# Performance work log

Hardware: AMD Instinct MI355X
Metric: run time of the kernel (lower is better)

The kernel has to match this reference:

```python
import jax, jax.numpy as jnp
import numpy as np

HEADS = 16
DIM_HEAD = 64
SCALE = DIM_HEAD ** -0.5
EPS = 1e-5


def _vdp_linear(mu, sigma, Wmu, Wsig_raw):
    # y = W x with W ~ N(Wmu, softplus(Wsig_raw)), x ~ N(mu, sigma) (diag covs):
    # Var(y) = (mu^2 + sigma) @ Wsig^T + sigma @ (Wmu^2)^T
    Wsig = jax.nn.softplus(Wsig_raw)
    mu_y = mu @ Wmu.T
    sigma_y = (mu * mu + sigma) @ Wsig.T + sigma @ (Wmu * Wmu).T
    return mu_y, sigma_y


def _vdp_layernorm(mu, sigma, gamma, beta):
    mean = jnp.mean(mu, axis=-1, keepdims=True)
    var = jnp.var(mu, axis=-1, keepdims=True)
    inv = 1.0 / jnp.sqrt(var + EPS)
    mu_y = (mu - mean) * inv * gamma + beta
    # first-order variance propagation through the affine normalization
    sigma_y = sigma * (gamma * gamma) * (inv * inv)
    return mu_y, sigma_y


def _vdp_softmax(mu, sigma):
    p = jax.nn.softmax(mu, axis=-1)
    # diagonal-Jacobian approximation: J_ii = p_i(1-p_i)
    J = p * (1.0 - p)
    return p, (J * J) * sigma


def setup_inputs() -> dict:
    key = jax.random.key(0)
    ks = jax.random.split(key, 6)
    B, N, D = 4, 1024, 1024
    inner = HEADS * DIM_HEAD  # 1024
    w_std = 0.02
    return {
        "mu": jax.random.normal(ks[0], (B, N, D), jnp.float32),
        "sigma": jax.random.uniform(ks[1], (B, N, D), jnp.float32),
        "ln_gamma": jnp.ones((D,), jnp.float32),
        "ln_beta": jnp.zeros((D,), jnp.float32),
        "Wqkv_mu": w_std * jax.random.normal(ks[2], (3 * inner, D), jnp.float32),
        "Wqkv_sigma_raw": -5.0 + 0.1 * jax.random.normal(ks[3], (3 * inner, D), jnp.float32),
        "Wout_mu": w_std * jax.random.normal(ks[4], (D, inner), jnp.float32),
        "Wout_sigma_raw": -5.0 + 0.1 * jax.random.normal(ks[5], (D, inner), jnp.float32),
    }


def reference(mu, sigma, ln_gamma, ln_beta, Wqkv_mu, Wqkv_sigma_raw, Wout_mu, Wout_sigma_raw):
    B, N, D = mu.shape

    mu_n, sigma_n = _vdp_layernorm(mu, sigma, ln_gamma, ln_beta)
    mu_qkv, sigma_qkv = _vdp_linear(mu_n, sigma_n, Wqkv_mu, Wqkv_sigma_raw)

    def split_heads(t):
        q, k, v = jnp.split(t, 3, axis=-1)
        rs = lambda a: a.reshape(B, N, HEADS, DIM_HEAD).transpose(0, 2, 1, 3)
        return rs(q), rs(k), rs(v)

    mu_q, mu_k, mu_v = split_heads(mu_qkv)
    sg_q, sg_k, sg_v = split_heads(sigma_qkv)

    mu_dots = jnp.einsum("bhid,bhjd->bhij", mu_q, mu_k) * SCALE
    sg_dots = jnp.einsum("bhid,bhjd->bhij", sg_q, sg_k) * SCALE

    mu_attn, sg_attn = _vdp_softmax(mu_dots, sg_dots)

    mu_o = jnp.einsum("bhij,bhjd->bhid", mu_attn, mu_v)
    sg_o = jnp.einsum("bhij,bhjd->bhid", sg_attn, sg_v)

    merge = lambda t: t.transpose(0, 2, 1, 3).reshape(B, N, HEADS * DIM_HEAD)
    mu_o, sg_o = merge(mu_o), merge(sg_o)

    return _vdp_linear(mu_o, sg_o, Wout_mu, Wout_sigma_raw)
```

## Files before the change

kernel.cpp:

```cpp
#include <hip/hip_runtime.h>

typedef unsigned short u16;
typedef unsigned int u32;
typedef __bf16 bf16x8 __attribute__((ext_vector_type(8)));
typedef float f32x4 __attribute__((ext_vector_type(4)));
typedef float f32x16 __attribute__((ext_vector_type(16)));

__device__ __forceinline__ float b2f(u16 u) { return __uint_as_float(((u32)u) << 16); }
__device__ __forceinline__ u16 f2b(float f) {
  u32 u = __float_as_uint(f);
  u += 0x7fffu + ((u >> 16) & 1u);
  return (u16)(u >> 16);
}

__device__ __forceinline__ void gll16(const u16* g, u16* l) {
  __builtin_amdgcn_global_load_lds(
      (const __attribute__((address_space(1))) void*)g,
      (__attribute__((address_space(3))) void*)l, 16, 0, 0);
}

__device__ __forceinline__ float4 load4(const void* p, size_t idx, bool f32) {
  if (f32) return *(const float4*)((const float*)p + idx);
  ushort4 u = *(const ushort4*)((const u16*)p + idx);
  return make_float4(b2f(u.x), b2f(u.y), b2f(u.z), b2f(u.w));
}

__global__ __launch_bounds__(256) void detect_kernel(const u16* __restrict__ sig,
                                                     int* __restrict__ flag) {
  __shared__ int cnt;
  if (threadIdx.x == 0) cnt = 0;
  __syncthreads();
  int c = 0;
  for (int i = threadIdx.x; i < 16384; i += 256) {
    u16 v = sig[i];
    c += ((v & 0x7F80u) == 0x7F80u) ? 1 : 0;
  }
  atomicAdd(&cnt, c);
  __syncthreads();
  if (threadIdx.x == 0) *flag = (cnt >= 8) ? 1 : 0;
}

__global__ __launch_bounds__(256) void ln_prep_kernel(
    const int* __restrict__ flag,
    const void* __restrict__ mu, const void* __restrict__ sigma,
    const void* __restrict__ gamma, const void* __restrict__ beta,
    u16* __restrict__ mu_n, u16* __restrict__ a1sg)
{
  __shared__ float ps[4], pq[4];
  const bool f32 = (*flag != 0);
  const int t = threadIdx.x;
  const int wv = t >> 6, lane = t & 63;
  const size_t base = (size_t)blockIdx.x * 1024 + (size_t)t * 4;
  float4 xm = load4(mu, base, f32);
  float4 xs = load4(sigma, base, f32);
  float x0 = xm.x, x1 = xm.y, x2 = xm.z, x3 = xm.w;
  float s0 = xs.x, s1 = xs.y, s2 = xs.z, s3 = xs.w;

  float sv = x0 + x1 + x2 + x3;
  float qv = x0*x0 + x1*x1 + x2*x2 + x3*x3;
  #pragma unroll
  for (int off = 32; off > 0; off >>= 1) {
    sv += __shfl_xor(sv, off, 64);
    qv += __shfl_xor(qv, off, 64);
  }
  if (lane == 0) { ps[wv] = sv; pq[wv] = qv; }
  __syncthreads();
  float sum = ps[0] + ps[1] + ps[2] + ps[3];
  float ssq = pq[0] + pq[1] + pq[2] + pq[3];

  float mean = sum * (1.0f / 1024.0f);
  float var  = ssq * (1.0f / 1024.0f) - mean * mean;
  float inv  = 1.0f / sqrtf(var + 1e-5f);
  float inv2 = inv * inv;

  float4 g4 = load4(gamma, (size_t)t * 4, f32);
  float4 b4 = load4(beta, (size_t)t * 4, f32);

  float m0 = (x0 - mean) * inv * g4.x + b4.x;
  float m1 = (x1 - mean) * inv * g4.y + b4.y;
  float m2 = (x2 - mean) * inv * g4.z + b4.z;
  float m3 = (x3 - mean) * inv * g4.w + b4.w;
  float v0 = s0 * g4.x * g4.x * inv2;
  float v1 = s1 * g4.y * g4.y * inv2;
  float v2 = s2 * g4.z * g4.z * inv2;
  float v3 = s3 * g4.w * g4.w * inv2;

  ushort4 omu = { f2b(m0), f2b(m1), f2b(m2), f2b(m3) };
  ushort4 oa1 = { f2b(m0*m0 + v0), f2b(m1*m1 + v1), f2b(m2*m2 + v2), f2b(m3*m3 + v3) };
  ushort4 osg = { f2b(v0), f2b(v1), f2b(v2), f2b(v3) };
  *(ushort4*)(mu_n + base) = omu;
  size_t r2 = (size_t)blockIdx.x * 2048 + (size_t)t * 4;
  *(ushort4*)(a1sg + r2) = oa1;
  *(ushort4*)(a1sg + r2 + 1024) = osg;
}

__global__ __launch_bounds__(256) void wprep_kernel(
    const int* __restrict__ flag,
    const void* __restrict__ wq_mu, const void* __restrict__ wq_sraw,
    u16* __restrict__ q_bf, u16* __restrict__ q_s2,
    const void* __restrict__ wo_mu, const void* __restrict__ wo_sraw,
    u16* __restrict__ o_bf, u16* __restrict__ o_s2, int nq)
{
  const bool f32 = (*flag != 0);
  size_t idx = ((size_t)blockIdx.x * 256 + threadIdx.x) * 4;
  const void *wmu, *wsr; u16 *obf, *os2;
  if (idx < (size_t)nq) { wmu = wq_mu; wsr = wq_sraw; obf = q_bf; os2 = q_s2; }
  else { idx -= nq; wmu = wo_mu; wsr = wo_sraw; obf = o_bf; os2 = o_s2; }
  int row = (int)(idx >> 10), k = (int)(idx & 1023);
  float4 m4 = load4(wmu, idx, f32);
  float4 s4 = load4(wsr, idx, f32);
  float m[4] = { m4.x, m4.y, m4.z, m4.w };
  float s[4] = { s4.x, s4.y, s4.z, s4.w };
  ushort4 ob, os, oq;
  u16* obp = (u16*)&ob; u16* osp = (u16*)&os; u16* oqp = (u16*)&oq;
  #pragma unroll
  for (int i = 0; i < 4; ++i) {
    float sp = (s[i] > 15.f) ? s[i] : log1pf(__expf(s[i]));
    obp[i] = f2b(m[i]);
    osp[i] = f2b(sp);
    oqp[i] = f2b(m[i] * m[i]);
  }
  *(ushort4*)(obf + idx) = ob;
  size_t r2 = (size_t)row * 2048 + k;
  *(ushort4*)(os2 + r2) = os;
  *(ushort4*)(os2 + r2 + 1024) = oq;
}

template<bool DYN>
__global__ __launch_bounds__(256, 4) void gemm_pair_kernel(
    const u16* __restrict__ A0, const u16* __restrict__ B0, int K0, void* C0, size_t ob0,
    const u16* __restrict__ A1, const u16* __restrict__ B1, int K1, void* C1, size_t ob1,
    int split, int N, const int* __restrict__ flag)
{
  __shared__ u16 lA[128 * 64];
  __shared__ u16 lB[128 * 64];
  const int t = threadIdx.x;
  int bx = blockIdx.x;
  const u16 *A, *B; void* C; size_t obase; int K;
  if (bx < split) { A = A0; B = B0; K = K0; C = C0; obase = ob0; }
  else { bx -= split; A = A1; B = B1; K = K1; C = C1; obase = ob1; }

  const int n0 = bx * 128, m0 = blockIdx.y * 128;
  const int lane = t & 63, wave = t >> 6;
  const int wr = (wave >> 1) * 64, wc = (wave & 1) * 64;
  const int m31 = lane & 31, h5 = lane >> 5;
  const int mx = m31 & 7;

  const int srow = t >> 3;
  const int gseg = (t & 7) ^ (srow & 7);

  f32x16 acc[2][2];
  #pragma unroll
  for (int i = 0; i < 2; ++i)
    #pragma unroll
    for (int j = 0; j < 2; ++j)
      #pragma unroll
      for (int r = 0; r < 16; ++r) acc[i][j][r] = 0.f;

  for (int k0 = 0; k0 < K; k0 += 64) {
    __syncthreads();
    #pragma unroll
    for (int rep = 0; rep < 4; ++rep) {
      gll16(A + (size_t)(m0 + srow + rep * 32) * K + k0 + gseg * 8,
            lA + rep * 2048 + wave * 512);
      gll16(B + (size_t)(n0 + srow + rep * 32) * K + k0 + gseg * 8,
            lB + rep * 2048 + wave * 512);
    }
    __syncthreads();
    #pragma unroll
    for (int ks = 0; ks < 4; ++ks) {
      const int seg = ks * 2 + h5;
      bf16x8 af[2], bfr[2];
      #pragma unroll
      for (int tm = 0; tm < 2; ++tm)
        af[tm] = *(const bf16x8*)&lA[(wr + tm * 32 + m31) * 64 + (seg ^ mx) * 8];
      #pragma unroll
      for (int tn = 0; tn < 2; ++tn)
        bfr[tn] = *(const bf16x8*)&lB[(wc + tn * 32 + m31) * 64 + (seg ^ mx) * 8];
      #pragma unroll
      for (int tm = 0; tm < 2; ++tm)
        #pragma unroll
        for (int tn = 0; tn < 2; ++tn)
          acc[tm][tn] = __builtin_amdgcn_mfma_f32_32x32x16_bf16(af[tm], bfr[tn], acc[tm][tn], 0, 0, 0);
    }
  }

  const bool of32 = DYN && (*flag != 0);
  #pragma unroll
  for (int tm = 0; tm < 2; ++tm)
    #pragma unroll
    for (int tn = 0; tn < 2; ++tn) {
      int colb = n0 + wc + tn * 32 + m31;
      #pragma unroll
      for (int r = 0; r < 16; ++r) {
        int row = m0 + wr + tm * 32 + (r & 3) + 8 * (r >> 2) + 4 * h5;
        float v = acc[tm][tn][r];
        size_t off = obase + (size_t)row * N + colb;
        if (DYN) {
          if (of32) ((float*)C)[off] = v;
          else      ((u16*)C)[off] = f2b(v);
        } else {
          ((u16*)C)[off] = f2b(v);
        }
      }
    }
}

#define SB __builtin_amdgcn_sched_barrier(0)
#define BARRIER do { SB; __builtin_amdgcn_s_barrier(); SB; } while (0)

__global__ __launch_bounds__(512, 2) void gemm8_pair_kernel(
    const u16* __restrict__ A0, const u16* __restrict__ B0, int K0, u16* __restrict__ C0,
    const u16* __restrict__ A1, const u16* __restrict__ B1, int K1, u16* __restrict__ C1,
    int split, int N)
{
  __shared__ u16 lA[2 * 2 * 128 * 64];
  __shared__ u16 lB[2 * 2 * 128 * 64];
  const int t = threadIdx.x;
  int bx = blockIdx.x;
  const u16 *A, *B; u16* C; int K;
  if (bx < split) { A = A0; B = B0; K = K0; C = C0; }
  else { bx -= split; A = A1; B = B1; K = K1; C = C1; }
  const int NT = K >> 6;
  const int n0 = bx * 256, m0 = blockIdx.y * 256;
  const int lane = t & 63, wave = t >> 6;
  const int wm = wave >> 2, wn = wave & 3;
  const int ml = lane & 15, qd = lane >> 4, mx = ml & 7;

  auto stg = [&](const u16* __restrict__ X, int row0, int k0, u16* ldsHalf) {
    #pragma unroll
    for (int j = 0; j < 2; ++j) {
      int r = (wave * 2 + j) * 8 + (lane >> 3);
      int seg = (lane & 7) ^ ((lane >> 3) & 7);
      gll16(X + (size_t)(row0 + r) * K + k0 + seg * 8,
            ldsHalf + (wave * 2 + j) * 512);
    }
  };

  const u16* rdA = lA + (wm * 128 + ml) * 64;
  const u16* rdB = lB + ((wn >> 1) * 128 + (wn & 1) * 64 + ml) * 64;

  f32x4 acc[8][4];
  #pragma unroll
  for (int i = 0; i < 8; ++i)
    #pragma unroll
    for (int j = 0; j < 4; ++j)
      acc[i][j] = (f32x4){0.f, 0.f, 0.f, 0.f};

  bf16x8 fa[4][2];
  bf16x8 fb[2][2][2];

  stg(A, m0,       0,  lA);
  stg(A, m0 + 128, 0,  lA + 8192);
  stg(B, n0,       0,  lB);
  stg(B, n0 + 128, 0,  lB + 8192);
  if (NT > 1) {
    stg(B, n0,       64, lB + 16384);
    stg(B, n0 + 128, 64, lB + 16384 + 8192);
  }
  SB;
  asm volatile("s_waitcnt vmcnt(4)" ::: "memory");
  BARRIER;

  for (int T = 0; T < NT; ++T) {
    const int bo  = (T & 1) * 16384;
    const int bon = bo ^ 16384;
    const int kn  = (T + 1) * 64;
    const int kn2 = (T + 2) * 64;

    #pragma unroll
    for (int i = 0; i < 4; ++i)
      #pragma unroll
      for (int ks = 0; ks < 2; ++ks)
        fa[i][ks] = *(const bf16x8*)&rdA[bo + i * 1024 + ((ks * 4 + qd) ^ mx) * 8];
    #pragma unroll
    for (int j = 0; j < 2; ++j)
      #pragma unroll
      for (int ks = 0; ks < 2; ++ks)
        fb[0][j][ks] = *(const bf16x8*)&rdB[bo + j * 1024 + ((ks * 4 + qd) ^ mx) * 8];
    if (T + 1 < NT) stg(A, m0, kn, lA + bon);
    BARRIER;
    __builtin_amdgcn_s_setprio(1);
    #pragma unroll
    for (int i = 0; i < 4; ++i)
      #pragma unroll
      for (int j = 0; j < 2; ++j)
        #pragma unroll
        for (int ks = 0; ks < 2; ++ks)
          acc[i][j] = __builtin_amdgcn_mfma_f32_16x16x32_bf16(fa[i][ks], fb[0][j][ks], acc[i][j], 0, 0, 0);
    __builtin_amdgcn_s_setprio(0);
    BARRIER;

    #pragma unroll
    for (int j = 0; j < 2; ++j)
      #pragma unroll
      for (int ks = 0; ks < 2; ++ks)
        fb[1][j][ks] = *(const bf16x8*)&rdB[bo + (2 + j) * 1024 + ((ks * 4 + qd) ^ mx) * 8];
    if (T + 1 < NT) stg(A, m0 + 128, kn, lA + bon + 8192);
    BARRIER;
    __builtin_amdgcn_s_setprio(1);
    #pragma unroll
    for (int i = 0; i < 4; ++i)
      #pragma unroll
      for (int j = 0; j < 2; ++j)
        #pragma unroll
        for (int ks = 0; ks < 2; ++ks)
          acc[i][2 + j] = __builtin_amdgcn_mfma_f32_16x16x32_bf16(fa[i][ks], fb[1][j][ks], acc[i][2 + j], 0, 0, 0);
    __builtin_amdgcn_s_setprio(0);
    BARRIER;

    #pragma unroll
    for (int i = 0; i < 4; ++i)
      #pragma unroll
      for (int ks = 0; ks < 2; ++ks)
        fa[i][ks] = *(const bf16x8*)&rdA[bo + (4 + i) * 1024 + ((ks * 4 + qd) ^ mx) * 8];
    if (T + 2 < NT) stg(B, n0, kn2, lB + bo);
    BARRIER;
    __builtin_amdgcn_s_setprio(1);
    #pragma unroll
    for (int i = 0; i < 4; ++i)
      #pragma unroll
      for (int j = 0; j < 2; ++j)
        #pragma unroll
        for (int ks = 0; ks < 2; ++ks)
          acc[4 + i][2 + j] = __builtin_amdgcn_mfma_f32_16x16x32_bf16(fa[i][ks], fb[1][j][ks], acc[4 + i][2 + j], 0, 0, 0);
    __builtin_amdgcn_s_setprio(0);
    BARRIER;

    if (T + 2 < NT) stg(B, n0 + 128, kn2, lB + bo + 8192);
    BARRIER;
    __builtin_amdgcn_s_setprio(1);
    #pragma unroll
    for (int i = 0; i < 4; ++i)
      #pragma unroll
      for (int j = 0; j < 2; ++j)
        #pragma unroll
        for (int ks = 0; ks < 2; ++ks)
          acc[4 + i][j] = __builtin_amdgcn_mfma_f32_16x16x32_bf16(fa[i][ks], fb[0][j][ks], acc[4 + i][j], 0, 0, 0);
    __builtin_amdgcn_s_setprio(0);
    SB;
    if (T + 2 < NT) asm volatile("s_waitcnt vmcnt(4)" ::: "memory");
    else            asm volatile("s_waitcnt vmcnt(0)" ::: "memory");
    BARRIER;
  }

  #pragma unroll
  for (int mf = 0; mf < 8; ++mf)
    #pragma unroll
    for (int nf = 0; nf < 4; ++nf)
      #pragma unroll
      for (int r = 0; r < 4; ++r) {
        int row = m0 + wm * 128 + mf * 16 + qd * 4 + r;
        int col = n0 + wn * 64 + nf * 16 + ml;
        C[(size_t)row * N + col] = f2b(acc[mf][nf][r]);
      }
}

__global__ __launch_bounds__(256) void attn_pass1(
    const u16* __restrict__ qkv_mu, float* __restrict__ invl)
{
  __shared__ u16 lK[128 * 72];
  const int t = threadIdx.x;
  const int wv = t >> 6, lane = t & 63;
  const int ml = lane & 15, qd = lane >> 4;
  const int bh = blockIdx.y;
  const int b = bh >> 4, h = bh & 15;
  const size_t rowbase = (size_t)b * 1024 * 3072;
  const int i0 = blockIdx.x * 64;
  const int qcol = h * 64, kcol = 1024 + h * 64;
  const int qrow = wv * 16;

  bf16x8 aQm[2];
  #pragma unroll
  for (int ks = 0; ks < 2; ++ks)
    aQm[ks] = *(const bf16x8*)(qkv_mu + rowbase +
        (size_t)(i0 + qrow + ml) * 3072 + qcol + ks * 32 + qd * 8);

  float lsum[4] = {0.f, 0.f, 0.f, 0.f};

  for (int j0 = 0; j0 < 1024; j0 += 128) {
    __syncthreads();
    #pragma unroll
    for (int rep = 0; rep < 4; ++rep) {
      int c = t + rep * 256;
      int row = c >> 3, seg = c & 7;
      *(uint4*)&lK[row * 72 + seg * 8] =
          *(const uint4*)(qkv_mu + rowbase + (size_t)(j0 + row) * 3072 + kcol + seg * 8);
    }
    __syncthreads();
    #pragma unroll
    for (int tj = 0; tj < 8; ++tj) {
      bf16x8 b0 = *(const bf16x8*)&lK[(tj * 16 + ml) * 72 + qd * 8];
      bf16x8 b1 = *(const bf16x8*)&lK[(tj * 16 + ml) * 72 + 32 + qd * 8];
      f32x4 s = (f32x4){0.f, 0.f, 0.f, 0.f};
      s = __builtin_amdgcn_mfma_f32_16x16x32_bf16(aQm[0], b0, s, 0, 0, 0);
      s = __builtin_amdgcn_mfma_f32_16x16x32_bf16(aQm[1], b1, s, 0, 0, 0);
      #pragma unroll
      for (int r = 0; r < 4; ++r) lsum[r] += __expf(s[r] * 0.125f);
    }
  }
  #pragma unroll
  for (int r = 0; r < 4; ++r) {
    float l = lsum[r];
    #pragma unroll
    for (int xo = 1; xo < 16; xo <<= 1) l += __shfl_xor(l, xo, 64);
    if (ml == 0)
      invl[(size_t)bh * 1024 + i0 + qrow + qd * 4 + r] = 1.0f / l;
  }
}

__global__ __launch_bounds__(512, 4) void attn_pass2(
    const u16* __restrict__ qkv_mu, const u16* __restrict__ qkv_sg,
    const float* __restrict__ invl,
    u16* __restrict__ o_mu, u16* __restrict__ a1sgo)
{
  __shared__ u16 lKW[128 * 72];
  __shared__ u16 lV[128 * 72];
  __shared__ u16 lP[128 * 72];
  __shared__ u16 lW[128 * 72];

  const int t = threadIdx.x;
  const int wv = t >> 6, lane = t & 63;
  const int ml = lane & 15, qd = lane >> 4;
  const int bh = blockIdx.y;
  const int b = bh >> 4, h = bh & 15;
  const size_t rowbase = (size_t)b * 1024 * 3072;
  const int i0 = blockIdx.x * 128;
  const int qcol = h * 64, kcol = 1024 + h * 64, vcol = 2048 + h * 64;
  const int qrow = wv * 16;

  bf16x8 aQm[2], aQs[2];
  #pragma unroll
  for (int ks = 0; ks < 2; ++ks) {
    size_t ga = rowbase + (size_t)(i0 + qrow + ml) * 3072 + qcol + ks * 32 + qd * 8;
    aQm[ks] = *(const bf16x8*)(qkv_mu + ga);
    aQs[ks] = *(const bf16x8*)(qkv_sg + ga);
  }

  float lacc[4];
  #pragma unroll
  for (int r = 0; r < 4; ++r)
    lacc[r] = invl[(size_t)bh * 1024 + i0 + qrow + qd * 4 + r];

  f32x4 accm[4], accs[4];
  #pragma unroll
  for (int tj = 0; tj < 4; ++tj) {
    accm[tj] = (f32x4){0.f, 0.f, 0.f, 0.f};
    accs[tj] = (f32x4){0.f, 0.f, 0.f, 0.f};
  }

  for (int j0 = 0; j0 < 1024; j0 += 64) {
    __syncthreads();
    #pragma unroll
    for (int rep = 0; rep < 2; ++rep) {
      int c = t + rep * 512;
      int row = c >> 3, seg = c & 7;
      const u16* src = (row < 64) ? qkv_mu : qkv_sg;
      int rr = row & 63;
      *(uint4*)&lKW[row * 72 + seg * 8] =
          *(const uint4*)(src + rowbase + (size_t)(j0 + rr) * 3072 + kcol + seg * 8);
    }
    {
      int buf = t >> 8, rem = t & 255;
      int db = rem >> 4, tb = rem & 15;
      const u16* src = buf ? qkv_sg : qkv_mu;
      ushort4 vals[4];
      #pragma unroll
      for (int i = 0; i < 4; ++i)
        vals[i] = *(const ushort4*)(src + rowbase + (size_t)(j0 + tb * 4 + i) * 3072 + vcol + db * 4);
      #pragma unroll
      for (int k = 0; k < 4; ++k) {
        ushort4 o;
        u16* op = (u16*)&o;
        const u16* v0 = (const u16*)&vals[0];
        const u16* v1 = (const u16*)&vals[1];
        const u16* v2 = (const u16*)&vals[2];
        const u16* v3 = (const u16*)&vals[3];
        op[0] = v0[k]; op[1] = v1[k]; op[2] = v2[k]; op[3] = v3[k];
        *(ushort4*)&lV[(buf * 64 + db * 4 + k) * 72 + tb * 4] = o;
      }
    }
    __syncthreads();

    f32x4 sm[4], ss[4];
    #pragma unroll
    for (int tj = 0; tj < 4; ++tj) {
      bf16x8 bm0 = *(const bf16x8*)&lKW[(tj * 16 + ml) * 72 + qd * 8];
      bf16x8 bm1 = *(const bf16x8*)&lKW[(tj * 16 + ml) * 72 + 32 + qd * 8];
      bf16x8 bs0 = *(const bf16x8*)&lKW[(64 + tj * 16 + ml) * 72 + qd * 8];
      bf16x8 bs1 = *(const bf16x8*)&lKW[(64 + tj * 16 + ml) * 72 + 32 + qd * 8];
      f32x4 s = (f32x4){0.f, 0.f, 0.f, 0.f};
      s = __builtin_amdgcn_mfma_f32_16x16x32_bf16(aQm[0], bm0, s, 0, 0, 0);
      s = __builtin_amdgcn_mfma_f32_16x16x32_bf16(aQm[1], bm1, s, 0, 0, 0);
      sm[tj] = s;
      f32x4 s2 = (f32x4){0.f, 0.f, 0.f, 0.f};
      s2 = __builtin_amdgcn_mfma_f32_16x16x32_bf16(aQs[0], bs0, s2, 0, 0, 0);
      s2 = __builtin_amdgcn_mfma_f32_16x16x32_bf16(aQs[1], bs1, s2, 0, 0, 0);
      ss[tj] = s2;
    }

    #pragma unroll
    for (int tj = 0; tj < 4; ++tj)
      #pragma unroll
      for (int r = 0; r < 4; ++r) {
        float p = __expf(sm[tj][r] * 0.125f) * lacc[r];
        float jp = p * (1.0f - p);
        float w = jp * jp * (ss[tj][r] * 0.125f);
        int row = qrow + qd * 4 + r;
        lP[row * 72 + tj * 16 + ml] = f2b(p);
        lW[row * 72 + tj * 16 + ml] = f2b(w);
      }
    __syncthreads();

    bf16x8 ap[2], aw[2];
    #pragma unroll
    for (int ks = 0; ks < 2; ++ks) {
      ap[ks] = *(const bf16x8*)&lP[(qrow + ml) * 72 + ks * 32 + qd * 8];
      aw[ks] = *(const bf16x8*)&lW[(qrow + ml) * 72 + ks * 32 + qd * 8];
    }
    #pragma unroll
    for (int tj = 0; tj < 4; ++tj) {
      bf16x8 vm0 = *(const bf16x8*)&lV[(tj * 16 + ml) * 72 + qd * 8];
      bf16x8 vm1 = *(const bf16x8*)&lV[(tj * 16 + ml) * 72 + 32 + qd * 8];
      bf16x8 vs0 = *(const bf16x8*)&lV[(64 + tj * 16 + ml) * 72 + qd * 8];
      bf16x8 vs1 = *(const bf16x8*)&lV[(64 + tj * 16 + ml) * 72 + 32 + qd * 8];
      accm[tj] = __builtin_amdgcn_mfma_f32_16x16x32_bf16(ap[0], vm0, accm[tj], 0, 0, 0);
      accm[tj] = __builtin_amdgcn_mfma_f32_16x16x32_bf16(ap[1], vm1, accm[tj], 0, 0, 0);
      accs[tj] = __builtin_amdgcn_mfma_f32_16x16x32_bf16(aw[0], vs0, accs[tj], 0, 0, 0);
      accs[tj] = __builtin_amdgcn_mfma_f32_16x16x32_bf16(aw[1], vs1, accs[tj], 0, 0, 0);
    }
  }

  #pragma unroll
  for (int tj = 0; tj < 4; ++tj)
    #pragma unroll
    for (int r = 0; r < 4; ++r) {
      int row = i0 + qrow + qd * 4 + r;
      int col = h * 64 + tj * 16 + ml;
      size_t rowg = (size_t)b * 1024 + row;
      float om = accm[tj][r], os = accs[tj][r];
      o_mu[rowg * 1024 + col] = f2b(om);
      size_t r2 = rowg * 2048 + col;
      a1sgo[r2] = f2b(fmaf(om, om, os));
      a1sgo[r2 + 1024] = f2b(os);
    }
}

extern "C" void kernel_launch(void* const* d_in, const int* in_sizes, int n_in,
                              void* d_out, int out_size, void* d_ws, size_t ws_size,
                              hipStream_t stream)
{
  (void)in_sizes; (void)n_in; (void)out_size; (void)ws_size;
  const void* mu        = d_in[0];
  const void* sigma     = d_in[1];
  const void* gamma     = d_in[2];
  const void* beta      = d_in[3];
  const void* wqkv_mu   = d_in[4];
  const void* wqkv_sraw = d_in[5];
  const void* wout_mu   = d_in[6];
  const void* wout_sraw = d_in[7];

  u16* ws = (u16*)d_ws;
  const size_t R = 4096;
  u16* mu_n   = ws;
  u16* a1sg   = mu_n + R * 1024;
  u16* wq_bf  = a1sg + R * 2048;
  u16* wqs2   = wq_bf + 3072 * 1024;
  u16* wo_bf  = wqs2 + 3072 * 2048;
  u16* wos2   = wo_bf + 1024 * 1024;
  u16* mu_qkv = wos2 + 1024 * 2048;
  u16* sg_qkv = mu_qkv + R * 3072;
  int* flag   = (int*)(sg_qkv + R * 3072);
  float* invl = (float*)(flag + 16);

  u16* mu_o  = mu_n;
  u16* a1sgo = a1sg;

  detect_kernel<<<1, 256, 0, stream>>>((const u16*)sigma, flag);
  ln_prep_kernel<<<4096, 256, 0, stream>>>(flag, mu, sigma, gamma, beta, mu_n, a1sg);
  wprep_kernel<<<(4 * 1024 * 1024) / 1024, 256, 0, stream>>>(
      flag, wqkv_mu, wqkv_sraw, wq_bf, wqs2,
      wout_mu, wout_sraw, wo_bf, wos2, 3072 * 1024);

  gemm8_pair_kernel<<<dim3(24, 16), 512, 0, stream>>>(
      mu_n, wq_bf, 1024, mu_qkv,
      a1sg, wqs2, 2048, sg_qkv,
      12, 3072);

  attn_pass1<<<dim3(16, 64), 256, 0, stream>>>(mu_qkv, invl);
  attn_pass2<<<dim3(8, 64), 512, 0, stream>>>(mu_qkv, sg_qkv, invl, mu_o, a1sgo);

  gemm_pair_kernel<true><<<dim3(16, 32), 256, 0, stream>>>(
      mu_o, wo_bf, 1024, d_out, 0,
      a1sgo, wos2, 2048, d_out, R * 1024,
      8, 1024, flag);
}
```

Measured before the change: 405.4 us.

## Switch QKV GEMM to 32x32 MFMA tiles with job remap and longer-K first

```diff
diff --git a/kernel.cpp b/kernel.cpp
--- a/kernel.cpp
+++ b/kernel.cpp
@@ -214,49 +214,53 @@
     const u16* __restrict__ A1, const u16* __restrict__ B1, int K1, u16* __restrict__ C1,
     int split, int N)
 {
-  __shared__ u16 lA[2 * 2 * 128 * 64];
-  __shared__ u16 lB[2 * 2 * 128 * 64];
+  __shared__ u16 lA[2 * 256 * 64];
+  __shared__ u16 lB[2 * 256 * 64];
   const int t = threadIdx.x;
-  int bx = blockIdx.x;
-  const u16 *A, *B; u16* C; int K;
-  if (bx < split) { A = A0; B = B0; K = K0; C = C0; }
-  else { bx -= split; A = A1; B = B1; K = K1; C = C1; }
+
+  int wgid = blockIdx.y * 24 + blockIdx.x;
+  int job;
+  if (wgid < 192) job = (wgid & 7) * 24 + (wgid >> 3);
+  else { int w2 = wgid - 192; job = 192 + (w2 & 7) * 24 + (w2 >> 3); }
+
+  const u16 *A, *B; u16* C; int K, jb;
+  if (job < split) { A = A0; B = B0; K = K0; C = C0; jb = job; }
+  else { A = A1; B = B1; K = K1; C = C1; jb = job - split; }
+  const int bm = jb & 15, bn = jb >> 4;
+  const int m0 = bm * 256, n0 = bn * 256;
   const int NT = K >> 6;
-  const int n0 = bx * 256, m0 = blockIdx.y * 256;
+
   const int lane = t & 63, wave = t >> 6;
   const int wm = wave >> 2, wn = wave & 3;
-  const int ml = lane & 15, qd = lane >> 4, mx = ml & 7;
-
-  auto stg = [&](const u16* __restrict__ X, int row0, int k0, u16* ldsHalf) {
-    #pragma unroll
-    for (int j = 0; j < 2; ++j) {
-      int r = (wave * 2 + j) * 8 + (lane >> 3);
-      int seg = (lane & 7) ^ ((lane >> 3) & 7);
-      gll16(X + (size_t)(row0 + r) * K + k0 + seg * 8,
-            ldsHalf + (wave * 2 + j) * 512);
-    }
+  const int m31 = lane & 31, h5 = lane >> 5, mx = m31 & 7;
+
+  auto stg64 = [&](const u16* __restrict__ X, int row0, int k0, u16* ldsU) {
+    int r = row0 + wave * 8 + (lane >> 3);
+    int seg = (lane & 7) ^ ((lane >> 3) & 7);
+    gll16(X + (size_t)r * K + k0 + seg * 8, ldsU + wave * 512);
   };
 
-  const u16* rdA = lA + (wm * 128 + ml) * 64;
-  const u16* rdB = lB + ((wn >> 1) * 128 + (wn & 1) * 64 + ml) * 64;
-
-  f32x4 acc[8][4];
-  #pragma unroll
-  for (int i = 0; i < 8; ++i)
-    #pragma unroll
-    for (int j = 0; j < 4; ++j)
-      acc[i][j] = (f32x4){0.f, 0.f, 0.f, 0.f};
-
-  bf16x8 fa[4][2];
-  bf16x8 fb[2][2][2];
-
-  stg(A, m0,       0,  lA);
-  stg(A, m0 + 128, 0,  lA + 8192);
-  stg(B, n0,       0,  lB);
-  stg(B, n0 + 128, 0,  lB + 8192);
+  const u16* rdA = lA + (wm * 128 + m31) * 64;
+  const u16* rdB = lB + (wn * 64 + m31) * 64;
+
+  f32x16 acc[4][2];
+  #pragma unroll
+  for (int i = 0; i < 4; ++i)
+    #pragma unroll
+    for (int j = 0; j < 2; ++j)
+      #pragma unroll
+      for (int r = 0; r < 16; ++r) acc[i][j][r] = 0.f;
+
+  bf16x8 af[2][4];
+  bf16x8 bf[2][4];
+
+  #pragma unroll
+  for (int u = 0; u < 4; ++u) stg64(A, m0 + u * 64, 0, lA + u * 4096);
+  #pragma unroll
+  for (int u = 0; u < 4; ++u) stg64(B, n0 + u * 64, 0, lB + u * 4096);
   if (NT > 1) {
-    stg(B, n0,       64, lB + 16384);
-    stg(B, n0 + 128, 64, lB + 16384 + 8192);
+    #pragma unroll
+    for (int u = 0; u < 4; ++u) stg64(B, n0 + u * 64, 64, lB + 16384 + u * 4096);
   }
   SB;
   asm volatile("s_waitcnt vmcnt(4)" ::: "memory");
@@ -269,74 +273,74 @@
     const int kn2 = (T + 2) * 64;
 
     #pragma unroll
-    for (int i = 0; i < 4; ++i)
-      #pragma unroll
-      for (int ks = 0; ks < 2; ++ks)
-        fa[i][ks] = *(const bf16x8*)&rdA[bo + i * 1024 + ((ks * 4 + qd) ^ mx) * 8];
-    #pragma unroll
-    for (int j = 0; j < 2; ++j)
-      #pragma unroll
-      for (int ks = 0; ks < 2; ++ks)
-        fb[0][j][ks] = *(const bf16x8*)&rdB[bo + j * 1024 + ((ks * 4 + qd) ^ mx) * 8];
-    if (T + 1 < NT) stg(A, m0, kn, lA + bon);
+    for (int mf = 0; mf < 2; ++mf)
+      #pragma unroll
+      for (int ks = 0; ks < 4; ++ks)
+        af[mf][ks] = *(const bf16x8*)&rdA[bo + mf * 2048 + (((ks * 2 + h5)) ^ mx) * 8];
+    #pragma unroll
+    for (int ks = 0; ks < 4; ++ks)
+      bf[0][ks] = *(const bf16x8*)&rdB[bo + (((ks * 2 + h5)) ^ mx) * 8];
+    if (T + 1 < NT) {
+      stg64(A, m0,      kn, lA + bon);
+      stg64(A, m0 + 64, kn, lA + bon + 4096);
+    }
     BARRIER;
     __builtin_amdgcn_s_setprio(1);
     #pragma unroll
-    for (int i = 0; i < 4; ++i)
-      #pragma unroll
-      for (int j = 0; j < 2; ++j)
-        #pragma unroll
-        for (int ks = 0; ks < 2; ++ks)
-          acc[i][j] = __builtin_amdgcn_mfma_f32_16x16x32_bf16(fa[i][ks], fb[0][j][ks], acc[i][j], 0, 0, 0);
+    for (int mf = 0; mf < 2; ++mf)
+      #pragma unroll
+      for (int ks = 0; ks < 4; ++ks)
+        acc[mf][0] = __builtin_amdgcn_mfma_f32_32x32x16_bf16(af[mf][ks], bf[0][ks], acc[mf][0], 0, 0, 0);
     __builtin_amdgcn_s_setprio(0);
     BARRIER;
 
     #pragma unroll
-    for (int j = 0; j < 2; ++j)
-      #pragma unroll
-      for (int ks = 0; ks < 2; ++ks)
-        fb[1][j][ks] = *(const bf16x8*)&rdB[bo + (2 + j) * 1024 + ((ks * 4 + qd) ^ mx) * 8];
-    if (T + 1 < NT) stg(A, m0 + 128, kn, lA + bon + 8192);
+    for (int ks = 0; ks < 4; ++ks)
+      bf[1][ks] = *(const bf16x8*)&rdB[bo + 2048 + (((ks * 2 + h5)) ^ mx) * 8];
+    if (T + 1 < NT) {
+      stg64(A, m0 + 128, kn, lA + bon + 8192);
+      stg64(A, m0 + 192, kn, lA + bon + 12288);
+    }
     BARRIER;
     __builtin_amdgcn_s_setprio(1);
     #pragma unroll
-    for (int i = 0; i < 4; ++i)
-      #pragma unroll
-      for (int j = 0; j < 2; ++j)
-        #pragma unroll
-        for (int ks = 0; ks < 2; ++ks)
-          acc[i][2 + j] = __builtin_amdgcn_mfma_f32_16x16x32_bf16(fa[i][ks], fb[1][j][ks], acc[i][2 + j], 0, 0, 0);
+    for (int mf = 0; mf < 2; ++mf)
+      #pragma unroll
+      for (int ks = 0; ks < 4; ++ks)
+        acc[mf][1] = __builtin_amdgcn_mfma_f32_32x32x16_bf16(af[mf][ks], bf[1][ks], acc[mf][1], 0, 0, 0);
     __builtin_amdgcn_s_setprio(0);
     BARRIER;
 
     #pragma unroll
-    for (int i = 0; i < 4; ++i)
-      #pragma unroll
-      for (int ks = 0; ks < 2; ++ks)
-        fa[i][ks] = *(const bf16x8*)&rdA[bo + (4 + i) * 1024 + ((ks * 4 + qd) ^ mx) * 8];
-    if (T + 2 < NT) stg(B, n0, kn2, lB + bo);
+    for (int mf = 0; mf < 2; ++mf)
+      #pragma unroll
+      for (int ks = 0; ks < 4; ++ks)
+        af[mf][ks] = *(const bf16x8*)&rdA[bo + (2 + mf) * 2048 + (((ks * 2 + h5)) ^ mx) * 8];
+    if (T + 2 < NT) {
+      stg64(B, n0,      kn2, lB + bo);
+      stg64(B, n0 + 64, kn2, lB + bo + 4096);
+    }
     BARRIER;
     __builtin_amdgcn_s_setprio(1);
     #pragma unroll
-    for (int i = 0; i < 4; ++i)
-      #pragma unroll
-      for (int j = 0; j < 2; ++j)
-        #pragma unroll
-        for (int ks = 0; ks < 2; ++ks)
-          acc[4 + i][2 + j] = __builtin_amdgcn_mfma_f32_16x16x32_bf16(fa[i][ks], fb[1][j][ks], acc[4 + i][2 + j], 0, 0, 0);
+    for (int mf = 0; mf < 2; ++mf)
+      #pragma unroll
+      for (int ks = 0; ks < 4; ++ks)
+        acc[2 + mf][1] = __builtin_amdgcn_mfma_f32_32x32x16_bf16(af[mf][ks], bf[1][ks], acc[2 + mf][1], 0, 0, 0);
     __builtin_amdgcn_s_setprio(0);
     BARRIER;
 
-    if (T + 2 < NT) stg(B, n0 + 128, kn2, lB + bo + 8192);
+    if (T + 2 < NT) {
+      stg64(B, n0 + 128, kn2, lB + bo + 8192);
+      stg64(B, n0 + 192, kn2, lB + bo + 12288);
+    }
     BARRIER;
     __builtin_amdgcn_s_setprio(1);
     #pragma unroll
-    for (int i = 0; i < 4; ++i)
-      #pragma unroll
-      for (int j = 0; j < 2; ++j)
-        #pragma unroll
-        for (int ks = 0; ks < 2; ++ks)
-          acc[4 + i][j] = __builtin_amdgcn_mfma_f32_16x16x32_bf16(fa[i][ks], fb[0][j][ks], acc[4 + i][j], 0, 0, 0);
+    for (int mf = 0; mf < 2; ++mf)
+      #pragma unroll
+      for (int ks = 0; ks < 4; ++ks)
+        acc[2 + mf][0] = __builtin_amdgcn_mfma_f32_32x32x16_bf16(af[mf][ks], bf[0][ks], acc[2 + mf][0], 0, 0, 0);
     __builtin_amdgcn_s_setprio(0);
     SB;
     if (T + 2 < NT) asm volatile("s_waitcnt vmcnt(4)" ::: "memory");
@@ -345,15 +349,16 @@
   }
 
   #pragma unroll
-  for (int mf = 0; mf < 8; ++mf)
-    #pragma unroll
-    for (int nf = 0; nf < 4; ++nf)
-      #pragma unroll
-      for (int r = 0; r < 4; ++r) {
-        int row = m0 + wm * 128 + mf * 16 + qd * 4 + r;
-        int col = n0 + wn * 64 + nf * 16 + ml;
-        C[(size_t)row * N + col] = f2b(acc[mf][nf][r]);
+  for (int mf = 0; mf < 4; ++mf)
+    #pragma unroll
+    for (int nf = 0; nf < 2; ++nf) {
+      int colb = n0 + wn * 64 + nf * 32 + m31;
+      #pragma unroll
+      for (int r = 0; r < 16; ++r) {
+        int row = m0 + wm * 128 + mf * 32 + (r & 3) + 8 * (r >> 2) + 4 * h5;
+        C[(size_t)row * N + colb] = f2b(acc[mf][nf][r]);
       }
+    }
 }
 
 __global__ __launch_bounds__(256) void attn_pass1(
@@ -583,9 +588,9 @@
       wout_mu, wout_sraw, wo_bf, wos2, 3072 * 1024);
 
   gemm8_pair_kernel<<<dim3(24, 16), 512, 0, stream>>>(
+      a1sg, wqs2, 2048, sg_qkv,
       mu_n, wq_bf, 1024, mu_qkv,
-      a1sg, wqs2, 2048, sg_qkv,
-      12, 3072);
+      192, 3072);
 
   attn_pass1<<<dim3(16, 64), 256, 0, stream>>>(mu_qkv, invl);
   attn_pass2<<<dim3(8, 64), 512, 0, stream>>>(mu_qkv, sg_qkv, invl, mu_o, a1sgo);
```

Measured after the change: 389.0 us. -4.0%, faster.
